# Performance work log

Measured on AMD Instinct MI355X. Metric: run time of the kernel, lower is better.

The kernel has to match this reference:

```python
import jax, jax.numpy as jnp
import numpy as np

K = 2  # number of propagation hops (SGConv K)


def setup_inputs() -> dict:
    key = jax.random.key(0)
    k1, k2, k3 = jax.random.split(key, 3)
    N, F, C, E = 100000, 64, 40, 1200000
    x = jax.random.normal(k1, (N, F), dtype=jnp.float32)
    edge_index = jax.random.randint(k2, (2, E), 0, N, dtype=jnp.int64)
    W = jax.random.normal(k3, (C, F), dtype=jnp.float32) * (1.0 / np.sqrt(F))
    b = jnp.zeros((C,), dtype=jnp.float32)
    return {"x": x, "edge_index": edge_index, "W": W, "b": b}


def reference(x, edge_index, W, b):
    N = x.shape[0]
    # add self-loops (PyG gcn_norm with add_self_loops=True)
    loop = jnp.arange(N, dtype=edge_index.dtype)
    src = jnp.concatenate([edge_index[0], loop])  # message sources j
    dst = jnp.concatenate([edge_index[1], loop])  # aggregation targets i
    # symmetric normalization: deg over targets, norm_e = d_src^-1/2 * d_dst^-1/2
    deg = jax.ops.segment_sum(jnp.ones_like(src, dtype=x.dtype), dst, num_segments=N)
    dinv = jnp.where(deg > 0, jax.lax.rsqrt(deg), 0.0)
    norm = dinv[src] * dinv[dst]  # [E+N]
    # K-hop propagation: x <- scatter_add(norm * x[src]) at dst
    for _ in range(K):
        x = jax.ops.segment_sum(x[src] * norm[:, None], dst, num_segments=N)
    logits = x @ W.T + b  # [N, C]
    return jax.nn.log_softmax(logits, axis=1)
```

## Files before the change

### kernel.cpp

```cpp
#include <hip/hip_runtime.h>
#include <math.h>

#define FDIM 64
#define CPAD 64
#define NPB  256
#define CAP2B 3456
#define NBMAX 400
#define TILE2 2048
#define EPT2 8
#define PTILE 128


__device__ inline unsigned short f2bf(float f) {
    unsigned int u = __float_as_uint(f);
    unsigned int r = (u + 0x7fffu + ((u >> 16) & 1u)) >> 16;
    return (unsigned short)r;
}
__device__ inline float bf_lo(unsigned int v) { return __uint_as_float(v << 16); }
__device__ inline float bf_hi(unsigned int v) { return __uint_as_float(v & 0xffff0000u); }
__device__ inline unsigned int bfpack(float a, float b) {
    return (unsigned int)f2bf(a) | ((unsigned int)f2bf(b) << 16);
}

__global__ __launch_bounds__(256) void k_zero(int* __restrict__ p, int n) {
    int i = blockIdx.x * 256 + threadIdx.x;
    if (i < n) p[i] = 0;
}


__global__ __launch_bounds__(256) void k_binD(const int* __restrict__ src,
                                              const int* __restrict__ dst,
                                              int* __restrict__ bcnt,
                                              unsigned int* __restrict__ bin2,
                                              int E, int NB) {
    __shared__ int hb[NBMAX];
    __shared__ int hc[NBMAX];
    int tid = threadIdx.x;
    int base = blockIdx.x * TILE2;
    for (int i = tid; i < NB; i += 256) { hb[i] = 0; hc[i] = 0; }
    __syncthreads();
    unsigned int ent[EPT2]; int bk[EPT2];
#pragma unroll
    for (int k = 0; k < EPT2; ++k) {
        int i = base + k * 256 + tid;
        if (i < E) {
            int s = src[i], d = dst[i];
            bk[k] = d >> 8;
            ent[k] = ((unsigned int)s << 8) | (unsigned int)(d & 255);
            atomicAdd(&hb[bk[k]], 1);
        } else bk[k] = -1;
    }
    __syncthreads();
    for (int i = tid; i < NB; i += 256) {
        int c = hb[i];
        hb[i] = (c > 0) ? atomicAdd(&bcnt[i], c) : 0;
    }
    __syncthreads();
#pragma unroll
    for (int k = 0; k < EPT2; ++k) if (bk[k] >= 0) {
        int b = bk[k];
        int pos = hb[b] + atomicAdd(&hc[b], 1);
        if (pos < CAP2B) bin2[(size_t)b * CAP2B + pos] = ent[k];
    }
}


__global__ __launch_bounds__(512) void k_bscan(const int* __restrict__ bcnt,
                                               int* __restrict__ cbase,
                                               int* __restrict__ row_ptr,
                                               int NB, int N, int T) {
    __shared__ int lds[512];
    int tid = threadIdx.x;
    int tot = 0;
    if (tid < NB)
        tot = min(bcnt[tid], CAP2B) + min(NPB, N - tid * NPB);
    lds[tid] = tot;
    __syncthreads();
    int val = tot;
#pragma unroll
    for (int off = 1; off < 512; off <<= 1) {
        int o = (tid >= off) ? lds[tid - off] : 0;
        __syncthreads();
        val += o;
        lds[tid] = val;
        __syncthreads();
    }
    if (tid < NB) cbase[tid] = val - tot;
    if (tid == 0) row_ptr[N] = T;
}

__global__ __launch_bounds__(256) void k_build(const int* __restrict__ bcnt,
                                               const int* __restrict__ cbase,
                                               const unsigned int* __restrict__ bin2,
                                               int* __restrict__ row_ptr,
                                               float* __restrict__ dinv,
                                               int* __restrict__ csr_src, int N) {
    __shared__ int lcnt[256];
    __shared__ int lscan[256];
    __shared__ int lbase[256];
    __shared__ int lcur[256];
    int b = blockIdx.x, tid = threadIdx.x;
    int node = (b << 8) + tid;
    lcnt[tid] = (node < N) ? 1 : 0;
    __syncthreads();
    int M = min(bcnt[b], CAP2B);
    const unsigned int* seg = bin2 + (size_t)b * CAP2B;
    for (int i = tid; i < M; i += 256)
        atomicAdd(&lcnt[seg[i] & 255u], 1);
    __syncthreads();
    int v = lcnt[tid];
    lscan[tid] = v;
    __syncthreads();
    int val = v;
#pragma unroll
    for (int off = 1; off < 256; off <<= 1) {
        int o = (tid >= off) ? lscan[tid - off] : 0;
        __syncthreads();
        val += o;
        lscan[tid] = val;
        __syncthreads();
    }
    int base = cbase[b] + (val - v);
    if (node < N) {
        row_ptr[node] = base;
        dinv[node] = rsqrtf((float)v);
        csr_src[base] = node;
    }
    lbase[tid] = base;
    lcur[tid] = 1;
    __syncthreads();
    for (int i = tid; i < M; i += 256) {
        unsigned int en = seg[i];
        int dl = (int)(en & 255u);
        int pos = lbase[dl] + atomicAdd(&lcur[dl], 1);
        csr_src[pos] = (int)(en >> 8);
    }
}


__global__ __launch_bounds__(256) void k_proj(const float* __restrict__ x,
                                              const float* __restrict__ W,
                                              const float* __restrict__ dinv,
                                              unsigned short* __restrict__ p16,
                                              int N, int C) {
    __shared__ float xs[PTILE][65];
    __shared__ float Wl[40 * 65];
    int tid = threadIdx.x;
    int n0 = blockIdx.x * PTILE;

    for (int i = tid; i < 40 * 64; i += 256) {
        int c = i >> 6, f = i & 63;
        Wl[c * 65 + f] = W[i];
    }
    for (int idx = tid; idx < PTILE * 16; idx += 256) {
        int r = idx >> 4, c4 = (idx & 15) << 2;
        int n = n0 + r;
        float4 v = make_float4(0.f, 0.f, 0.f, 0.f);
        float dn = 0.f;
        if (n < N) {
            v = *(const float4*)&x[(size_t)n * FDIM + c4];
            dn = dinv[n];
        }
        xs[r][c4 + 0] = v.x * dn; xs[r][c4 + 1] = v.y * dn;
        xs[r][c4 + 2] = v.z * dn; xs[r][c4 + 3] = v.w * dn;
    }
    __syncthreads();

    int ng = tid & 31;
    int cg = tid >> 5;
    float acc[4][5];
#pragma unroll
    for (int i = 0; i < 4; ++i)
#pragma unroll
        for (int j = 0; j < 5; ++j) acc[i][j] = 0.f;

#pragma unroll 4
    for (int k = 0; k < FDIM; ++k) {
        float xv[4], wv[5];
#pragma unroll
        for (int i = 0; i < 4; ++i) xv[i] = xs[ng + 32 * i][k];
#pragma unroll
        for (int j = 0; j < 5; ++j) wv[j] = Wl[(cg * 5 + j) * 65 + k];
#pragma unroll
        for (int i = 0; i < 4; ++i)
#pragma unroll
            for (int j = 0; j < 5; ++j)
                acc[i][j] = fmaf(xv[i], wv[j], acc[i][j]);
    }
    __syncthreads();

    unsigned short* ps = (unsigned short*)xs;
#pragma unroll
    for (int i = 0; i < 4; ++i) {
        int r = ng + 32 * i;
#pragma unroll
        for (int j = 0; j < 5; ++j)
            ps[r * 64 + cg * 5 + j] = f2bf(acc[i][j]);
    }
    for (int idx = tid; idx < PTILE * 24; idx += 256) {
        int r = idx / 24, c = 40 + idx % 24;
        ps[r * 64 + c] = 0;
    }
    __syncthreads();
    const unsigned int* pu = (const unsigned int*)ps;
    unsigned int* po = (unsigned int*)p16;
    for (int idx = tid; idx < PTILE * 32; idx += 256) {
        int r = idx >> 5;
        int n = n0 + r;
        if (n < N) po[(size_t)n * 32 + (idx & 31)] = pu[idx];
    }
}


__global__ __launch_bounds__(256) void k_hop1(const int* __restrict__ row_ptr,
                                              const int* __restrict__ csr_src,
                                              const float* __restrict__ dinv,
                                              const uint4* __restrict__ pin4,
                                              uint4* __restrict__ yout4,
                                              int N) {
    int g = threadIdx.x >> 3;
    int t = threadIdx.x & 7;
    int node = blockIdx.x * 32 + g;
    if (node >= N) return;
    int beg = row_ptr[node], end = row_ptr[node + 1];

    float a0 = 0.f, a1 = 0.f, a2 = 0.f, a3 = 0.f;
    float a4 = 0.f, a5 = 0.f, a6 = 0.f, a7 = 0.f;
    for (int e0 = beg; e0 < end; e0 += 4) {
        int si[4]; uint4 vs[4];
#pragma unroll
        for (int k = 0; k < 4; ++k) {
            int idx = e0 + k;
            si[k] = (idx < end) ? csr_src[idx] : -1;
        }
#pragma unroll
        for (int k = 0; k < 4; ++k)
            if (si[k] >= 0) vs[k] = pin4[si[k] * 8 + t];
#pragma unroll
        for (int k = 0; k < 4; ++k)
            if (si[k] >= 0) {
                a0 += bf_lo(vs[k].x); a1 += bf_hi(vs[k].x);
                a2 += bf_lo(vs[k].y); a3 += bf_hi(vs[k].y);
                a4 += bf_lo(vs[k].z); a5 += bf_hi(vs[k].z);
                a6 += bf_lo(vs[k].w); a7 += bf_hi(vs[k].w);
            }
    }
    float dn = dinv[node], sc = dn * dn;
    yout4[node * 8 + t] = make_uint4(bfpack(a0 * sc, a1 * sc),
                                     bfpack(a2 * sc, a3 * sc),
                                     bfpack(a4 * sc, a5 * sc),
                                     bfpack(a6 * sc, a7 * sc));
}


__global__ __launch_bounds__(256) void k_hop2_lsm(const int* __restrict__ row_ptr,
                                                  const int* __restrict__ csr_src,
                                                  const float* __restrict__ dinv,
                                                  const uint4* __restrict__ pin4,
                                                  const float* __restrict__ bias,
                                                  float* __restrict__ out,
                                                  int N, int C) {
    __shared__ float bl[64];
    int tid = threadIdx.x;
    if (tid < 64) bl[tid] = (tid < C) ? bias[tid] : 0.f;
    __syncthreads();

    int g = tid >> 3;
    int t = tid & 7;
    int node = blockIdx.x * 32 + g;
    if (node >= N) return;
    int beg = row_ptr[node], end = row_ptr[node + 1];

    float a[8];
#pragma unroll
    for (int j = 0; j < 8; ++j) a[j] = 0.f;
    for (int e0 = beg; e0 < end; e0 += 4) {
        int si[4]; uint4 vs[4];
#pragma unroll
        for (int k = 0; k < 4; ++k) {
            int idx = e0 + k;
            si[k] = (idx < end) ? csr_src[idx] : -1;
        }
#pragma unroll
        for (int k = 0; k < 4; ++k)
            if (si[k] >= 0) vs[k] = pin4[si[k] * 8 + t];
#pragma unroll
        for (int k = 0; k < 4; ++k)
            if (si[k] >= 0) {
                a[0] += bf_lo(vs[k].x); a[1] += bf_hi(vs[k].x);
                a[2] += bf_lo(vs[k].y); a[3] += bf_hi(vs[k].y);
                a[4] += bf_lo(vs[k].z); a[5] += bf_hi(vs[k].z);
                a[6] += bf_lo(vs[k].w); a[7] += bf_hi(vs[k].w);
            }
    }

    float dn = dinv[node];
    int c0 = 8 * t;
    bool valid = (c0 < C);
    float l[8];
#pragma unroll
    for (int j = 0; j < 8; ++j)
        l[j] = valid ? fmaf(a[j], dn, bl[c0 + j]) : -INFINITY;

    float m = l[0];
#pragma unroll
    for (int j = 1; j < 8; ++j) m = fmaxf(m, l[j]);
    m = fmaxf(m, __shfl_xor(m, 1));
    m = fmaxf(m, __shfl_xor(m, 2));
    m = fmaxf(m, __shfl_xor(m, 4));

    float s = 0.f;
    if (valid) {
#pragma unroll
        for (int j = 0; j < 8; ++j) s += expf(l[j] - m);
    }
    s += __shfl_xor(s, 1);
    s += __shfl_xor(s, 2);
    s += __shfl_xor(s, 4);
    float ls = m + logf(s);

    if (valid) {
        float* op = out + (size_t)node * C + c0;
        float4 r0 = make_float4(l[0] - ls, l[1] - ls, l[2] - ls, l[3] - ls);
        float4 r1 = make_float4(l[4] - ls, l[5] - ls, l[6] - ls, l[7] - ls);
        *(float4*)op = r0;
        *(float4*)(op + 4) = r1;
    }
}


extern "C" void kernel_launch(void* const* d_in, const int* in_sizes, int n_in,
                              void* d_out, int out_size, void* d_ws, size_t ws_size,
                              hipStream_t stream) {
    const float* x  = (const float*)d_in[0];
    const int*   ei = (const int*)d_in[1];
    const float* W  = (const float*)d_in[2];
    const float* b  = (const float*)d_in[3];
    float* out = (float*)d_out;

    const int C = in_sizes[3];
    const int F = in_sizes[2] / C;
    const int N = in_sizes[0] / F;
    const int E = in_sizes[1] / 2;
    (void)F;

    const int* src = ei;
    const int* dst = ei + E;
    const int T  = E + N;
    const int NB = (N + NPB - 1) / NPB;

    char* w8 = (char*)d_ws;
    auto alloc = [&](size_t bytes) {
        char* p = w8;
        w8 += (bytes + 255) & ~(size_t)255;
        return p;
    };
    int*   bcnt    = (int*)  alloc((size_t)NB * 4);
    int*   cbase   = (int*)  alloc((size_t)NB * 4);
    int*   row_ptr = (int*)  alloc((size_t)(N + 1) * 4);
    float* dinv    = (float*)alloc((size_t)N * 4);
    unsigned int* bin2 = (unsigned int*)alloc((size_t)NB * CAP2B * 4);
    int*   csr_src = (int*)  alloc((size_t)T * 4);
    unsigned short* p16 = (unsigned short*)alloc((size_t)N * CPAD * 2);
    uint4* y16     = (uint4*)alloc((size_t)N * 8 * 16);

    const int B = 256;
    const int NT = (E + TILE2 - 1) / TILE2;

    k_zero <<<(NB + B - 1) / B, B, 0, stream>>>(bcnt, NB);
    k_binD <<<NT, B, 0, stream>>>(src, dst, bcnt, bin2, E, NB);
    k_bscan<<<1, 512, 0, stream>>>(bcnt, cbase, row_ptr, NB, N, T);
    k_build<<<NB, B, 0, stream>>>(bcnt, cbase, bin2, row_ptr, dinv, csr_src, N);

    k_proj <<<(N + PTILE - 1) / PTILE, B, 0, stream>>>(x, W, dinv, p16, N, C);

    k_hop1 <<<(N + 31) / 32, B, 0, stream>>>(row_ptr, csr_src, dinv,
                                             (const uint4*)p16, y16, N);

    k_hop2_lsm<<<(N + 31) / 32, B, 0, stream>>>(row_ptr, csr_src, dinv,
                                                (const uint4*)y16, b, out, N, C);
}
```

Before: 130.1 us.

## Split projected features into 64B+16B arrays and use 4 lanes per node

Replaces the 64-channel padded bf16 projection buffer (128B per node) with two arrays: 32 channels in a 64-byte array and the remaining 8 channels in a 16-byte array. This removes the 24 padding channels from every gather in both hops, cutting gathered bytes per edge, and packs 64 nodes per block with 4 lanes each. The tail array is handled by lane 0 only, which adds divergence and an extra dependent load per edge for that lane, and splits each gathered row across two cache-line regions.

Result: no change. 131.7 us (+1.2%).

```diff
diff --git a/kernel.cpp b/kernel.cpp
--- a/kernel.cpp
+++ b/kernel.cpp
@@ -2,7 +2,6 @@
 #include <math.h>
 
 #define FDIM 64
-#define CPAD 64
 #define NPB  256
 #define CAP2B 3456
 #define NBMAX 400
@@ -141,7 +140,8 @@
 __global__ __launch_bounds__(256) void k_proj(const float* __restrict__ x,
                                               const float* __restrict__ W,
                                               const float* __restrict__ dinv,
-                                              unsigned short* __restrict__ p16,
+                                              unsigned int* __restrict__ pA,
+                                              unsigned int* __restrict__ pB,
                                               int N, int C) {
     __shared__ float xs[PTILE][65];
     __shared__ float Wl[40 * 65];
@@ -197,17 +197,17 @@
         for (int j = 0; j < 5; ++j)
             ps[r * 64 + cg * 5 + j] = f2bf(acc[i][j]);
     }
-    for (int idx = tid; idx < PTILE * 24; idx += 256) {
-        int r = idx / 24, c = 40 + idx % 24;
-        ps[r * 64 + c] = 0;
-    }
     __syncthreads();
     const unsigned int* pu = (const unsigned int*)ps;
-    unsigned int* po = (unsigned int*)p16;
-    for (int idx = tid; idx < PTILE * 32; idx += 256) {
-        int r = idx >> 5;
+    for (int idx = tid; idx < PTILE * 16; idx += 256) {
+        int r = idx >> 4, u = idx & 15;
         int n = n0 + r;
-        if (n < N) po[(size_t)n * 32 + (idx & 31)] = pu[idx];
+        if (n < N) pA[n * 16 + u] = pu[r * 32 + u];
+    }
+    for (int idx = tid; idx < PTILE * 4; idx += 256) {
+        int r = idx >> 2, u = idx & 3;
+        int n = n0 + r;
+        if (n < N) pB[n * 4 + u] = pu[r * 32 + 16 + u];
     }
 }
 
@@ -215,19 +215,23 @@
 __global__ __launch_bounds__(256) void k_hop1(const int* __restrict__ row_ptr,
                                               const int* __restrict__ csr_src,
                                               const float* __restrict__ dinv,
-                                              const uint4* __restrict__ pin4,
-                                              uint4* __restrict__ yout4,
+                                              const uint4* __restrict__ pA4,
+                                              const uint4* __restrict__ pB4,
+                                              uint4* __restrict__ yA4,
+                                              uint4* __restrict__ yB4,
                                               int N) {
-    int g = threadIdx.x >> 3;
-    int t = threadIdx.x & 7;
-    int node = blockIdx.x * 32 + g;
+    int g = threadIdx.x >> 2;
+    int t = threadIdx.x & 3;
+    int node = blockIdx.x * 64 + g;
     if (node >= N) return;
     int beg = row_ptr[node], end = row_ptr[node + 1];
 
-    float a0 = 0.f, a1 = 0.f, a2 = 0.f, a3 = 0.f;
-    float a4 = 0.f, a5 = 0.f, a6 = 0.f, a7 = 0.f;
+    float a[8], bb[8];
+#pragma unroll
+    for (int j = 0; j < 8; ++j) { a[j] = 0.f; bb[j] = 0.f; }
+
     for (int e0 = beg; e0 < end; e0 += 4) {
-        int si[4]; uint4 vs[4];
+        int si[4]; uint4 vA[4], vB[4];
 #pragma unroll
         for (int k = 0; k < 4; ++k) {
             int idx = e0 + k;
@@ -235,28 +239,45 @@
         }
 #pragma unroll
         for (int k = 0; k < 4; ++k)
-            if (si[k] >= 0) vs[k] = pin4[si[k] * 8 + t];
+            if (si[k] >= 0) vA[k] = pA4[si[k] * 4 + t];
+#pragma unroll
+        for (int k = 0; k < 4; ++k)
+            if (si[k] >= 0 && t == 0) vB[k] = pB4[si[k]];
 #pragma unroll
         for (int k = 0; k < 4; ++k)
             if (si[k] >= 0) {
-                a0 += bf_lo(vs[k].x); a1 += bf_hi(vs[k].x);
-                a2 += bf_lo(vs[k].y); a3 += bf_hi(vs[k].y);
-                a4 += bf_lo(vs[k].z); a5 += bf_hi(vs[k].z);
-                a6 += bf_lo(vs[k].w); a7 += bf_hi(vs[k].w);
+                a[0] += bf_lo(vA[k].x); a[1] += bf_hi(vA[k].x);
+                a[2] += bf_lo(vA[k].y); a[3] += bf_hi(vA[k].y);
+                a[4] += bf_lo(vA[k].z); a[5] += bf_hi(vA[k].z);
+                a[6] += bf_lo(vA[k].w); a[7] += bf_hi(vA[k].w);
             }
+#pragma unroll
+        for (int k = 0; k < 4; ++k)
+            if (si[k] >= 0 && t == 0) {
+                bb[0] += bf_lo(vB[k].x); bb[1] += bf_hi(vB[k].x);
+                bb[2] += bf_lo(vB[k].y); bb[3] += bf_hi(vB[k].y);
+                bb[4] += bf_lo(vB[k].z); bb[5] += bf_hi(vB[k].z);
+                bb[6] += bf_lo(vB[k].w); bb[7] += bf_hi(vB[k].w);
+            }
     }
     float dn = dinv[node], sc = dn * dn;
-    yout4[node * 8 + t] = make_uint4(bfpack(a0 * sc, a1 * sc),
-                                     bfpack(a2 * sc, a3 * sc),
-                                     bfpack(a4 * sc, a5 * sc),
-                                     bfpack(a6 * sc, a7 * sc));
+    yA4[node * 4 + t] = make_uint4(bfpack(a[0] * sc, a[1] * sc),
+                                   bfpack(a[2] * sc, a[3] * sc),
+                                   bfpack(a[4] * sc, a[5] * sc),
+                                   bfpack(a[6] * sc, a[7] * sc));
+    if (t == 0)
+        yB4[node] = make_uint4(bfpack(bb[0] * sc, bb[1] * sc),
+                               bfpack(bb[2] * sc, bb[3] * sc),
+                               bfpack(bb[4] * sc, bb[5] * sc),
+                               bfpack(bb[6] * sc, bb[7] * sc));
 }
 
 
 __global__ __launch_bounds__(256) void k_hop2_lsm(const int* __restrict__ row_ptr,
                                                   const int* __restrict__ csr_src,
                                                   const float* __restrict__ dinv,
-                                                  const uint4* __restrict__ pin4,
+                                                  const uint4* __restrict__ pA4,
+                                                  const uint4* __restrict__ pB4,
                                                   const float* __restrict__ bias,
                                                   float* __restrict__ out,
                                                   int N, int C) {
@@ -265,17 +286,18 @@
     if (tid < 64) bl[tid] = (tid < C) ? bias[tid] : 0.f;
     __syncthreads();
 
-    int g = tid >> 3;
-    int t = tid & 7;
-    int node = blockIdx.x * 32 + g;
+    int g = tid >> 2;
+    int t = tid & 3;
+    int node = blockIdx.x * 64 + g;
     if (node >= N) return;
     int beg = row_ptr[node], end = row_ptr[node + 1];
 
-    float a[8];
-#pragma unroll
-    for (int j = 0; j < 8; ++j) a[j] = 0.f;
+    float a[8], bb[8];
+#pragma unroll
+    for (int j = 0; j < 8; ++j) { a[j] = 0.f; bb[j] = 0.f; }
+
     for (int e0 = beg; e0 < end; e0 += 4) {
-        int si[4]; uint4 vs[4];
+        int si[4]; uint4 vA[4], vB[4];
 #pragma unroll
         for (int k = 0; k < 4; ++k) {
             int idx = e0 + k;
@@ -283,48 +305,63 @@
         }
 #pragma unroll
         for (int k = 0; k < 4; ++k)
-            if (si[k] >= 0) vs[k] = pin4[si[k] * 8 + t];
+            if (si[k] >= 0) vA[k] = pA4[si[k] * 4 + t];
+#pragma unroll
+        for (int k = 0; k < 4; ++k)
+            if (si[k] >= 0 && t == 0) vB[k] = pB4[si[k]];
 #pragma unroll
         for (int k = 0; k < 4; ++k)
             if (si[k] >= 0) {
-                a[0] += bf_lo(vs[k].x); a[1] += bf_hi(vs[k].x);
-                a[2] += bf_lo(vs[k].y); a[3] += bf_hi(vs[k].y);
-                a[4] += bf_lo(vs[k].z); a[5] += bf_hi(vs[k].z);
-                a[6] += bf_lo(vs[k].w); a[7] += bf_hi(vs[k].w);
+                a[0] += bf_lo(vA[k].x); a[1] += bf_hi(vA[k].x);
+                a[2] += bf_lo(vA[k].y); a[3] += bf_hi(vA[k].y);
+                a[4] += bf_lo(vA[k].z); a[5] += bf_hi(vA[k].z);
+                a[6] += bf_lo(vA[k].w); a[7] += bf_hi(vA[k].w);
+            }
+#pragma unroll
+        for (int k = 0; k < 4; ++k)
+            if (si[k] >= 0 && t == 0) {
+                bb[0] += bf_lo(vB[k].x); bb[1] += bf_hi(vB[k].x);
+                bb[2] += bf_lo(vB[k].y); bb[3] += bf_hi(vB[k].y);
+                bb[4] += bf_lo(vB[k].z); bb[5] += bf_hi(vB[k].z);
+                bb[6] += bf_lo(vB[k].w); bb[7] += bf_hi(vB[k].w);
             }
     }
 
     float dn = dinv[node];
     int c0 = 8 * t;
-    bool valid = (c0 < C);
-    float l[8];
-#pragma unroll
-    for (int j = 0; j < 8; ++j)
-        l[j] = valid ? fmaf(a[j], dn, bl[c0 + j]) : -INFINITY;
-
+    float l[8], lb[8];
+#pragma unroll
+    for (int j = 0; j < 8; ++j) l[j] = fmaf(a[j], dn, bl[c0 + j]);
     float m = l[0];
 #pragma unroll
     for (int j = 1; j < 8; ++j) m = fmaxf(m, l[j]);
+    if (t == 0) {
+#pragma unroll
+        for (int j = 0; j < 8; ++j) {
+            lb[j] = fmaf(bb[j], dn, bl[32 + j]);
+            m = fmaxf(m, lb[j]);
+        }
+    }
     m = fmaxf(m, __shfl_xor(m, 1));
     m = fmaxf(m, __shfl_xor(m, 2));
-    m = fmaxf(m, __shfl_xor(m, 4));
 
     float s = 0.f;
-    if (valid) {
-#pragma unroll
-        for (int j = 0; j < 8; ++j) s += expf(l[j] - m);
+#pragma unroll
+    for (int j = 0; j < 8; ++j) s += expf(l[j] - m);
+    if (t == 0) {
+#pragma unroll
+        for (int j = 0; j < 8; ++j) s += expf(lb[j] - m);
     }
     s += __shfl_xor(s, 1);
     s += __shfl_xor(s, 2);
-    s += __shfl_xor(s, 4);
     float ls = m + logf(s);
 
-    if (valid) {
-        float* op = out + (size_t)node * C + c0;
-        float4 r0 = make_float4(l[0] - ls, l[1] - ls, l[2] - ls, l[3] - ls);
-        float4 r1 = make_float4(l[4] - ls, l[5] - ls, l[6] - ls, l[7] - ls);
-        *(float4*)op = r0;
-        *(float4*)(op + 4) = r1;
+    float* op = out + (size_t)node * C;
+    *(float4*)(op + c0)     = make_float4(l[0] - ls, l[1] - ls, l[2] - ls, l[3] - ls);
+    *(float4*)(op + c0 + 4) = make_float4(l[4] - ls, l[5] - ls, l[6] - ls, l[7] - ls);
+    if (t == 0) {
+        *(float4*)(op + 32) = make_float4(lb[0] - ls, lb[1] - ls, lb[2] - ls, lb[3] - ls);
+        *(float4*)(op + 36) = make_float4(lb[4] - ls, lb[5] - ls, lb[6] - ls, lb[7] - ls);
     }
 }
 
@@ -361,8 +398,10 @@
     float* dinv    = (float*)alloc((size_t)N * 4);
     unsigned int* bin2 = (unsigned int*)alloc((size_t)NB * CAP2B * 4);
     int*   csr_src = (int*)  alloc((size_t)T * 4);
-    unsigned short* p16 = (unsigned short*)alloc((size_t)N * CPAD * 2);
-    uint4* y16     = (uint4*)alloc((size_t)N * 8 * 16);
+    unsigned int* pA = (unsigned int*)alloc((size_t)N * 16 * 4);
+    unsigned int* pB = (unsigned int*)alloc((size_t)N * 4 * 4);
+    unsigned int* yA = (unsigned int*)alloc((size_t)N * 16 * 4);
+    unsigned int* yB = (unsigned int*)alloc((size_t)N * 4 * 4);
 
     const int B = 256;
     const int NT = (E + TILE2 - 1) / TILE2;
@@ -372,11 +411,13 @@
     k_bscan<<<1, 512, 0, stream>>>(bcnt, cbase, row_ptr, NB, N, T);
     k_build<<<NB, B, 0, stream>>>(bcnt, cbase, bin2, row_ptr, dinv, csr_src, N);
 
-    k_proj <<<(N + PTILE - 1) / PTILE, B, 0, stream>>>(x, W, dinv, p16, N, C);
-
-    k_hop1 <<<(N + 31) / 32, B, 0, stream>>>(row_ptr, csr_src, dinv,
-                                             (const uint4*)p16, y16, N);
-
-    k_hop2_lsm<<<(N + 31) / 32, B, 0, stream>>>(row_ptr, csr_src, dinv,
-                                                (const uint4*)y16, b, out, N, C);
-}
+    k_proj <<<(N + PTILE - 1) / PTILE, B, 0, stream>>>(x, W, dinv, pA, pB, N, C);
+
+    k_hop1 <<<(N + 63) / 64, B, 0, stream>>>(row_ptr, csr_src, dinv,
+                                             (const uint4*)pA, (const uint4*)pB,
+                                             (uint4*)yA, (uint4*)yB, N);
+
+    k_hop2_lsm<<<(N + 63) / 64, B, 0, stream>>>(row_ptr, csr_src, dinv,
+                                                (const uint4*)yA, (const uint4*)yB,
+                                                b, out, N, C);
+}
```
